# Optimization experiments

Hardware: AMD Instinct MI355X
Metric: run time of the kernel (lower is better)

Reference implementation:

```python
import jax, jax.numpy as jnp
import numpy as np

B, S, H, NH, HD = 2, 2048, 2048, 16, 128
E, TOPK, I = 8, 2, 2048
EPS = 1e-5
ROPE_THETA = 10000.0


def setup_inputs() -> dict:
    key = jax.random.key(0)
    ks = jax.random.split(key, 11)
    s = 0.02
    return {
        "hidden_states": jax.random.normal(ks[0], (B, S, H), jnp.float32),
        "position_ids": jnp.broadcast_to(jnp.arange(S, dtype=jnp.int32), (B, S)),
        "rms1_w": jnp.ones((H,), jnp.float32),
        "rms2_w": jnp.ones((H,), jnp.float32),
        "q_w": jax.random.normal(ks[1], (H, H), jnp.float32) * s,
        "k_w": jax.random.normal(ks[2], (H, H), jnp.float32) * s,
        "v_w": jax.random.normal(ks[3], (H, H), jnp.float32) * s,
        "o_w": jax.random.normal(ks[4], (H, H), jnp.float32) * s,
        "router_w": jax.random.normal(ks[5], (H, E), jnp.float32) * s,
        "w1": jax.random.normal(ks[6], (E, H, I), jnp.float32) * s,
        "w2": jax.random.normal(ks[7], (E, I, H), jnp.float32) * s,
        "w3": jax.random.normal(ks[8], (E, H, I), jnp.float32) * s,
    }


def rmsnorm(x, w):
    var = jnp.mean(x * x, axis=-1, keepdims=True)
    return (x * jax.lax.rsqrt(var + EPS)) * w


def rope(x, pos):
    # x: [B,S,NH,HD], pos: [B,S]
    half = HD // 2
    inv_freq = 1.0 / (ROPE_THETA ** (jnp.arange(0, half, dtype=jnp.float32) / half))
    ang = pos.astype(jnp.float32)[..., None] * inv_freq  # [B,S,half]
    cos = jnp.cos(ang)[:, :, None, :]
    sin = jnp.sin(ang)[:, :, None, :]
    x1, x2 = x[..., :half], x[..., half:]
    return jnp.concatenate([x1 * cos - x2 * sin, x2 * cos + x1 * sin], axis=-1)


def attention(x, pos, q_w, k_w, v_w, o_w):
    q = (x @ q_w).reshape(B, S, NH, HD)
    k = (x @ k_w).reshape(B, S, NH, HD)
    v = (x @ v_w).reshape(B, S, NH, HD)
    q = rope(q, pos)
    k = rope(k, pos)
    scores = jnp.einsum("bqhd,bkhd->bhqk", q, k) / np.sqrt(HD).astype(np.float32)
    causal = jnp.tril(jnp.ones((S, S), bool))
    scores = jnp.where(causal, scores, jnp.finfo(scores.dtype).min)
    probs = jax.nn.softmax(scores, axis=-1)
    ctx = jnp.einsum("bhqk,bkhd->bqhd", probs, v).reshape(B, S, H)
    return ctx @ o_w


def moe(x, router_w, w1, w2, w3):
    t = x.reshape(B * S, H)
    probs = jax.nn.softmax(t @ router_w, axis=-1)  # [T,E]
    top_v, top_i = jax.lax.top_k(probs, TOPK)
    top_v = top_v / jnp.sum(top_v, axis=-1, keepdims=True)
    T = B * S
    coeff = jnp.zeros((T, E), x.dtype).at[jnp.arange(T)[:, None], top_i].set(top_v)
    y = jnp.zeros((T, H), x.dtype)
    for e in range(E):  # fixed small expert loop
        h = jax.nn.silu(t @ w1[e]) * (t @ w3[e])
        y = y + coeff[:, e:e + 1] * (h @ w2[e])
    return y.reshape(B, S, H)


def reference(hidden_states, position_ids, rms1_w, rms2_w, q_w, k_w, v_w, o_w,
              router_w, w1, w2, w3):
    residual = hidden_states
    h = rmsnorm(hidden_states, rms1_w).astype(hidden_states.dtype)
    h = attention(h, position_ids, q_w, k_w, v_w, o_w)
    h = residual + h
    residual = h
    h = rmsnorm(h, rms2_w).astype(h.dtype)
    h = moe(h, router_w, w1, w2, w3)
    return residual + h
```

## Files before the change

### kernel.cpp

```cpp
#include <hip/hip_runtime.h>
#include <hip/hip_bf16.h>

constexpr int CB   = 2;
constexpr int CS   = 2048;
constexpr int CH   = 2048;
constexpr int CNH  = 16;
constexpr int CHD  = 128;
constexpr int CE   = 8;
constexpr int CI   = 2048;
constexpr int CT   = CB * CS;
constexpr int CQKV = 3 * CH;

typedef __attribute__((ext_vector_type(8))) short short8;
typedef __attribute__((ext_vector_type(4))) float float4v;
typedef __attribute__((ext_vector_type(4))) unsigned short ushort4v;
typedef unsigned int uint32;

__device__ __forceinline__ float bf2f(unsigned short u) {
    union { unsigned int i; float f; } x; x.i = ((unsigned int)u) << 16; return x.f;
}
__device__ __forceinline__ unsigned short f2bf(float f) {
    union { float f; unsigned int i; } x; x.f = f;
    unsigned int r = x.i + 0x7fffu + ((x.i >> 16) & 1u);
    return (unsigned short)(r >> 16);
}
__device__ __forceinline__ uint32 packpair(uint32 r0, uint32 r1) {
    return __builtin_amdgcn_perm(r1, r0, 0x07060302u);
}
__device__ __forceinline__ uint32 rnebits(float f) {
    uint32 u = __float_as_uint(f);
    return u + 0x7fffu + ((u >> 16) & 1u);
}
__device__ __forceinline__ void split2(float f0, float f1, uint32& h, uint32& l) {
    uint32 r0 = rnebits(f0), r1 = rnebits(f1);
    h = packpair(r0, r1);
    float d0 = f0 - __uint_as_float(r0 & 0xffff0000u);
    float d1 = f1 - __uint_as_float(r1 & 0xffff0000u);
    l = packpair(rnebits(d0), rnebits(d1));
}
__device__ __forceinline__ void rne16_store(const float* fv, unsigned short* dst) {
    uint32 h[8];
    #pragma unroll
    for (int p = 0; p < 8; p++) h[p] = packpair(rnebits(fv[2 * p]), rnebits(fv[2 * p + 1]));
    ((uint4*)dst)[0] = make_uint4(h[0], h[1], h[2], h[3]);
    ((uint4*)dst)[1] = make_uint4(h[4], h[5], h[6], h[7]);
}
__device__ __forceinline__ void gl16(const void* g, void* l) {
    __builtin_amdgcn_global_load_lds(
        (const __attribute__((address_space(1))) void*)g,
        (__attribute__((address_space(3))) void*)l, 16, 0, 0);
}

__global__ __launch_bounds__(256) void rmsnorm_k(const float* __restrict__ x,
                                                 const float* __restrict__ w,
                                                 unsigned short* __restrict__ o1,
                                                 unsigned short* __restrict__ o2) {
    const int row = blockIdx.x;
    const float* xr = x + (size_t)row * CH;
    const int base = threadIdx.x * 8;
    float4 v0 = *(const float4*)(xr + base);
    float4 v1 = *(const float4*)(xr + base + 4);
    float ss = v0.x*v0.x + v0.y*v0.y + v0.z*v0.z + v0.w*v0.w
             + v1.x*v1.x + v1.y*v1.y + v1.z*v1.z + v1.w*v1.w;
    #pragma unroll
    for (int o = 1; o < 64; o <<= 1) ss += __shfl_xor(ss, o);
    __shared__ float ps[4];
    if ((threadIdx.x & 63) == 0) ps[threadIdx.x >> 6] = ss;
    __syncthreads();
    const float scale = rsqrtf((ps[0] + ps[1] + ps[2] + ps[3]) / (float)CH + 1e-5f);
    float4 w0 = *(const float4*)(w + base);
    float4 w1 = *(const float4*)(w + base + 4);
    float r[8] = {v0.x * scale * w0.x, v0.y * scale * w0.y, v0.z * scale * w0.z, v0.w * scale * w0.w,
                  v1.x * scale * w1.x, v1.y * scale * w1.y, v1.z * scale * w1.z, v1.w * scale * w1.w};
    uint32 h[4], l[4];
    #pragma unroll
    for (int p = 0; p < 4; p++) split2(r[2 * p], r[2 * p + 1], h[p], l[p]);
    *(uint4*)(o1 + (size_t)row * CH + base) = make_uint4(h[0], h[1], h[2], h[3]);
    *(uint4*)(o2 + (size_t)row * CH + base) = make_uint4(l[0], l[1], l[2], l[3]);
}

__global__ __launch_bounds__(256) void rmsrouter_k(const float* __restrict__ x,
                                                   const float* __restrict__ w,
                                                   const float* __restrict__ rw,
                                                   unsigned short* __restrict__ h2,
                                                   int* __restrict__ cnt,
                                                   int* __restrict__ tok,
                                                   float* __restrict__ gate) {
    const int row = blockIdx.x;
    const float* xr = x + (size_t)row * CH;
    const int base = threadIdx.x * 8;
    float4 v0 = *(const float4*)(xr + base);
    float4 v1 = *(const float4*)(xr + base + 4);
    float ss = v0.x*v0.x + v0.y*v0.y + v0.z*v0.z + v0.w*v0.w
             + v1.x*v1.x + v1.y*v1.y + v1.z*v1.z + v1.w*v1.w;
    #pragma unroll
    for (int o = 1; o < 64; o <<= 1) ss += __shfl_xor(ss, o);
    __shared__ float ps[4];
    __shared__ double dacc[4][8];
    const int wave = threadIdx.x >> 6, lane = threadIdx.x & 63;
    if (lane == 0) ps[wave] = ss;
    __syncthreads();
    const float scale = rsqrtf((ps[0] + ps[1] + ps[2] + ps[3]) / (float)CH + 1e-5f);
    float4 w0 = *(const float4*)(w + base);
    float4 w1 = *(const float4*)(w + base + 4);
    float r[8] = {v0.x * scale * w0.x, v0.y * scale * w0.y, v0.z * scale * w0.z, v0.w * scale * w0.w,
                  v1.x * scale * w1.x, v1.y * scale * w1.y, v1.z * scale * w1.z, v1.w * scale * w1.w};
    rne16_store(r, h2 + (size_t)row * CH + base);
    const float vv[8] = {v0.x, v0.y, v0.z, v0.w, v1.x, v1.y, v1.z, v1.w};
    const float ww[8] = {w0.x, w0.y, w0.z, w0.w, w1.x, w1.y, w1.z, w1.w};
    double acc[8] = {0, 0, 0, 0, 0, 0, 0, 0};
    #pragma unroll
    for (int jj = 0; jj < 8; jj++) {
        const double xn = (double)vv[jj] * (double)ww[jj];
        const float* rr = rw + (size_t)(base + jj) * CE;
        #pragma unroll
        for (int e = 0; e < 8; e++) acc[e] += xn * (double)rr[e];
    }
    #pragma unroll
    for (int e = 0; e < 8; e++) {
        #pragma unroll
        for (int o = 1; o < 64; o <<= 1) acc[e] += __shfl_xor(acc[e], o);
    }
    if (lane == 0) {
        #pragma unroll
        for (int e = 0; e < 8; e++) dacc[wave][e] = acc[e];
    }
    __syncthreads();
    if (threadIdx.x == 0) {
        double a[8];
        #pragma unroll
        for (int e = 0; e < 8; e++) a[e] = dacc[0][e] + dacc[1][e] + dacc[2][e] + dacc[3][e];
        int e0 = 0;
        #pragma unroll
        for (int e = 1; e < 8; e++) if (a[e] > a[e0]) e0 = e;
        int e1 = (e0 == 0) ? 1 : 0;
        #pragma unroll
        for (int e = 0; e < 8; e++) if (e != e0 && a[e] > a[e1]) e1 = e;
        const double dl = (double)scale * (a[e1] - a[e0]);
        const double p1r = exp(dl);
        const float g0 = (float)(1.0 / (1.0 + p1r));
        const float g1 = (float)(p1r / (1.0 + p1r));
        int pos0 = atomicAdd(&cnt[e0], 1);
        tok[e0 * 4096 + pos0] = row; gate[e0 * 4096 + pos0] = g0;
        int pos1 = atomicAdd(&cnt[e1], 1);
        tok[e1 * 4096 + pos1] = row; gate[e1 * 4096 + pos1] = g1;
    }
}

__global__ void rope_tab_k(float2* __restrict__ tab) {
    int i = blockIdx.x * 256 + threadIdx.x;
    int p = i >> 6, j = i & 63;
    double inv = pow(10000.0, -(double)j / 64.0);
    float invf = (float)inv;
    float angf = (float)p * invf;
    double da = (double)angf;
    tab[i] = make_float2((float)cos(da), (float)sin(da));
}

__global__ __launch_bounds__(256) void rope_k(unsigned short* __restrict__ qh,
                                              unsigned short* __restrict__ ql,
                                              const int* __restrict__ pos,
                                              const float2* __restrict__ tab) {
    int i = blockIdx.x * 256 + threadIdx.x;
    if (i >= CT * CNH * 8) return;
    int t = i >> 7, r = i & 127, hh = r >> 3, jo = (r & 7) << 3;
    const float2* tp = tab + (size_t)pos[t] * 64 + jo;
    float4 tc0 = ((const float4*)tp)[0];
    float4 tc1 = ((const float4*)tp)[1];
    float4 tc2 = ((const float4*)tp)[2];
    float4 tc3 = ((const float4*)tp)[3];
    float cx[8] = {tc0.x, tc0.z, tc1.x, tc1.z, tc2.x, tc2.z, tc3.x, tc3.z};
    float cy[8] = {tc0.y, tc0.w, tc1.y, tc1.w, tc2.y, tc2.w, tc3.y, tc3.w};
    const size_t off = (size_t)t * CQKV + hh * CHD + jo;
    #pragma unroll
    for (int s = 0; s < 2; s++) {
        unsigned short* hp = qh + off + s * CH;
        unsigned short* lp = ql + off + s * CH;
        short8 x1h = *(short8*)hp,        x1l = *(short8*)lp;
        short8 x2h = *(short8*)(hp + 64), x2l = *(short8*)(lp + 64);
        const unsigned short* p1h = (const unsigned short*)&x1h;
        const unsigned short* p1l = (const unsigned short*)&x1l;
        const unsigned short* p2h = (const unsigned short*)&x2h;
        const unsigned short* p2l = (const unsigned short*)&x2l;
        short8 y1h, y1l, y2h, y2l;
        unsigned short* q1h = (unsigned short*)&y1h;
        unsigned short* q1l = (unsigned short*)&y1l;
        unsigned short* q2h = (unsigned short*)&y2h;
        unsigned short* q2l = (unsigned short*)&y2l;
        #pragma unroll
        for (int jj = 0; jj < 8; jj++) {
            const float x1 = bf2f(p1h[jj]) + bf2f(p1l[jj]);
            const float x2 = bf2f(p2h[jj]) + bf2f(p2l[jj]);
            const float yy1 = x1 * cx[jj] - x2 * cy[jj];
            const float yy2 = x2 * cx[jj] + x1 * cy[jj];
            const uint32 r1 = rnebits(yy1), r2 = rnebits(yy2);
            q1h[jj] = (unsigned short)(r1 >> 16);
            q2h[jj] = (unsigned short)(r2 >> 16);
            q1l[jj] = f2bf(yy1 - __uint_as_float(r1 & 0xffff0000u));
            q2l[jj] = f2bf(yy2 - __uint_as_float(r2 & 0xffff0000u));
        }
        *(short8*)hp        = y1h;
        *(short8*)(hp + 64) = y2h;
        *(short8*)lp        = y1l;
        *(short8*)(lp + 64) = y2l;
    }
}

template<int NMAT>
__global__ __launch_bounds__(256) void conv_k(const float* __restrict__ S0,
                                              const float* __restrict__ S1,
                                              unsigned short* __restrict__ D) {
    __shared__ float t[64][65];
    const int n0 = blockIdx.x * 64, k0 = blockIdx.y * 64, e = blockIdx.z;
    const size_t esrc = (size_t)e * 2048 * 2048;
    const int cc = threadIdx.x & 63, r4 = threadIdx.x >> 6;
    const int nl = threadIdx.x >> 2, q = threadIdx.x & 3;
    #pragma unroll
    for (int s = 0; s < NMAT; s++) {
        const float* S = s ? S1 : S0;
        __syncthreads();
        #pragma unroll
        for (int j = 0; j < 16; j++) {
            const int row = j * 4 + r4;
            t[cc][row] = S[esrc + (size_t)(k0 + row) * 2048 + n0 + cc];
        }
        __syncthreads();
        const int orow = (NMAT == 2) ? (2 * (n0 + nl) + s) : (n0 + nl);
        unsigned short* dp = D + (size_t)e * (NMAT * 2048) * 2048 + (size_t)orow * 2048 + k0 + q * 16;
        float fv[16];
        #pragma unroll
        for (int j = 0; j < 16; j++) fv[j] = t[nl][q * 16 + j];
        rne16_store(fv, dp);
    }
}

template<int NMAT>
__global__ __launch_bounds__(256) void convs_k(const float* __restrict__ S0,
                                               const float* __restrict__ S1,
                                               const float* __restrict__ S2,
                                               unsigned short* __restrict__ Dh,
                                               unsigned short* __restrict__ Dl) {
    __shared__ float t[64][65];
    const int n0 = blockIdx.x * 64, k0 = blockIdx.y * 64, z = blockIdx.z;
    const float* S = S0;
    if (NMAT == 3) S = (z == 0) ? S0 : ((z == 1) ? S1 : S2);
    const int cc = threadIdx.x & 63, r4 = threadIdx.x >> 6;
    #pragma unroll
    for (int j = 0; j < 16; j++) {
        const int row = j * 4 + r4;
        t[cc][row] = S[(size_t)(k0 + row) * 2048 + n0 + cc];
    }
    __syncthreads();
    const int nl = threadIdx.x >> 2, q = threadIdx.x & 3;
    float fv[16];
    #pragma unroll
    for (int j = 0; j < 16; j++) fv[j] = t[nl][q * 16 + j];
    uint32 h[8], l[8];
    #pragma unroll
    for (int p = 0; p < 8; p++) split2(fv[2 * p], fv[2 * p + 1], h[p], l[p]);
    const size_t off = (size_t)(z * 2048 + n0 + nl) * 2048 + k0 + q * 16;
    ((uint4*)(Dh + off))[0] = make_uint4(h[0], h[1], h[2], h[3]);
    ((uint4*)(Dh + off))[1] = make_uint4(h[4], h[5], h[6], h[7]);
    ((uint4*)(Dl + off))[0] = make_uint4(l[0], l[1], l[2], l[3]);
    ((uint4*)(Dl + off))[1] = make_uint4(l[4], l[5], l[6], l[7]);
}

template<int MODE>
__global__ __launch_bounds__(256) void sgemm_k(
    const unsigned short* __restrict__ Ahg, const unsigned short* __restrict__ Alg, int lda,
    const unsigned short* __restrict__ Bhg, const unsigned short* __restrict__ Blg, int K,
    unsigned short* __restrict__ Ch, unsigned short* __restrict__ Cl,
    float* __restrict__ Cf, int ldc,
    const float* __restrict__ resid, float* __restrict__ C2) {
    __shared__ unsigned short SS[2][4][128 * 32];
    const int mt = blockIdx.x, nt = blockIdx.y, tid = threadIdx.x;
    const int m0 = mt * 128;
    const int wave = tid >> 6, lane = tid & 63;
    const int lr = lane & 15, lg = lane >> 4;
    const int wr = (tid >> 7) & 1, wc = (tid >> 6) & 1;
    const int sr = lane >> 2;
    const int sc = (lane & 3) * 8;
    const int r0 = wave * 32;
    const int lofs = r0 * 32;
    const unsigned short* gAh = Ahg + (size_t)(m0 + r0 + sr) * lda + sc;
    const unsigned short* gAl = Alg + (size_t)(m0 + r0 + sr) * lda + sc;
    const unsigned short* gBh = Bhg + (size_t)(nt * 128 + r0 + sr) * K + sc;
    const unsigned short* gBl = Blg + (size_t)(nt * 128 + r0 + sr) * K + sc;
    const size_t rstepA = (size_t)16 * lda, rstepB = (size_t)16 * K;

    float4v acc[4][4];
    #pragma unroll
    for (int m = 0; m < 4; m++)
        #pragma unroll
        for (int n = 0; n < 4; n++) acc[m][n] = (float4v){0.f, 0.f, 0.f, 0.f};

    gl16(gAh, &SS[0][0][lofs]);           gl16(gAh + rstepA, &SS[0][0][lofs + 512]);
    gl16(gAl, &SS[0][1][lofs]);           gl16(gAl + rstepA, &SS[0][1][lofs + 512]);
    gl16(gBh, &SS[0][2][lofs]);           gl16(gBh + rstepB, &SS[0][2][lofs + 512]);
    gl16(gBl, &SS[0][3][lofs]);           gl16(gBl + rstepB, &SS[0][3][lofs + 512]);
    __syncthreads();

    int cur = 0;
    for (int k0 = 0; k0 < K; k0 += 32) {
        if (k0 + 32 < K) {
            const int nb = cur ^ 1;
            const int kn = k0 + 32;
            gl16(gAh + kn, &SS[nb][0][lofs]);          gl16(gAh + kn + rstepA, &SS[nb][0][lofs + 512]);
            gl16(gAl + kn, &SS[nb][1][lofs]);          gl16(gAl + kn + rstepA, &SS[nb][1][lofs + 512]);
            gl16(gBh + kn, &SS[nb][2][lofs]);          gl16(gBh + kn + rstepB, &SS[nb][2][lofs + 512]);
            gl16(gBl + kn, &SS[nb][3][lofs]);          gl16(gBl + kn + rstepB, &SS[nb][3][lofs + 512]);
        }
        const unsigned short* PAh = SS[cur][0];
        const unsigned short* PAl = SS[cur][1];
        const unsigned short* PBh = SS[cur][2];
        const unsigned short* PBl = SS[cur][3];
        short8 fah[4], fal[4], fbh[4], fbl[4];
        #pragma unroll
        for (int m = 0; m < 4; m++) {
            fah[m] = *(const short8*)(PAh + (wr * 64 + m * 16 + lr) * 32 + lg * 8);
            fal[m] = *(const short8*)(PAl + (wr * 64 + m * 16 + lr) * 32 + lg * 8);
        }
        #pragma unroll
        for (int n = 0; n < 4; n++) {
            fbh[n] = *(const short8*)(PBh + (wc * 64 + n * 16 + lr) * 32 + lg * 8);
            fbl[n] = *(const short8*)(PBl + (wc * 64 + n * 16 + lr) * 32 + lg * 8);
        }
        #pragma unroll
        for (int n = 0; n < 4; n++)
            #pragma unroll
            for (int m = 0; m < 4; m++) {
                acc[m][n] = __builtin_amdgcn_mfma_f32_16x16x32_bf16(fal[m], fbh[n], acc[m][n], 0, 0, 0);
                acc[m][n] = __builtin_amdgcn_mfma_f32_16x16x32_bf16(fah[m], fbl[n], acc[m][n], 0, 0, 0);
                acc[m][n] = __builtin_amdgcn_mfma_f32_16x16x32_bf16(fah[m], fbh[n], acc[m][n], 0, 0, 0);
            }
        __syncthreads();
        cur ^= 1;
    }
    #pragma unroll
    for (int m = 0; m < 4; m++) {
        const int rb = wr * 64 + m * 16 + (lane >> 4) * 4;
        #pragma unroll
        for (int n = 0; n < 4; n++) {
            const int ccol = nt * 128 + wc * 64 + n * 16 + lr;
            #pragma unroll
            for (int r = 0; r < 4; r++) {
                const size_t idx = (size_t)(m0 + rb + r) * ldc + ccol;
                if (MODE == 1) {
                    const float v = acc[m][n][r] + resid[idx];
                    Cf[idx] = v;
                    C2[idx] = v;
                } else {
                    const float v = acc[m][n][r];
                    uint32 rr = rnebits(v);
                    Ch[idx] = (unsigned short)(rr >> 16);
                    Cl[idx] = f2bf(v - __uint_as_float(rr & 0xffff0000u));
                }
            }
        }
    }
}

template<int MODE>
__global__ __launch_bounds__(256) void gemm_k(
    const unsigned short* __restrict__ A, int lda,
    const unsigned short* __restrict__ Bt, int K, int Ne,
    void* __restrict__ Cp, int ldc,
    const int* __restrict__ cnt, const int* __restrict__ tokl,
    const float* __restrict__ gatel, const int* __restrict__ pb) {
    __shared__ unsigned short SS[2][2][128 * 32];
    const int nt = blockIdx.x, mt = blockIdx.y, e = blockIdx.z;
    const int m0 = mt * 128;
    const int c = cnt[e];
    if (m0 >= c) return;
    const int valid = (c - m0 < 128) ? (c - m0) : 128;
    const int tid = threadIdx.x;
    const int wave = tid >> 6, lane = tid & 63;
    const int lr = lane & 15;
    const int wr = (tid >> 7) & 1, wc = (tid >> 6) & 1;
    const int sr = lane >> 2, sc = (lane & 3) * 8;
    const int r0 = wave * 32;
    const int lofs = r0 * 32;
    size_t gr0, gr1;
    {
        int ra = r0 + sr, rb2 = r0 + 16 + sr;
        if (MODE == 2) {
            ra = ra < valid ? ra : valid - 1;
            rb2 = rb2 < valid ? rb2 : valid - 1;
            gr0 = (size_t)tokl[e * 4096 + m0 + ra];
            gr1 = (size_t)tokl[e * 4096 + m0 + rb2];
        } else {
            int x0 = m0 + ra, x1 = m0 + rb2;
            gr0 = (size_t)(pb[e] + (x0 < c ? x0 : c - 1));
            gr1 = (size_t)(pb[e] + (x1 < c ? x1 : c - 1));
        }
    }
    const unsigned short* gA0 = A + gr0 * (size_t)lda + sc;
    const unsigned short* gA1 = A + gr1 * (size_t)lda + sc;
    const unsigned short* gB = Bt + (size_t)e * Ne * K + (size_t)(nt * 128 + r0 + sr) * K + sc;
    const size_t rstepB = (size_t)16 * K;

    float4v acc[4][4];
    #pragma unroll
    for (int m = 0; m < 4; m++)
        #pragma unroll
        for (int n = 0; n < 4; n++) acc[m][n] = (float4v){0.f, 0.f, 0.f, 0.f};

    gl16(gA0, &SS[0][0][lofs]);           gl16(gA1, &SS[0][0][lofs + 512]);
    gl16(gB, &SS[0][1][lofs]);            gl16(gB + rstepB, &SS[0][1][lofs + 512]);
    __syncthreads();

    int cur = 0;
    for (int k0 = 0; k0 < K; k0 += 32) {
        if (k0 + 32 < K) {
            const int nb = cur ^ 1;
            const int kn = k0 + 32;
            gl16(gA0 + kn, &SS[nb][0][lofs]);          gl16(gA1 + kn, &SS[nb][0][lofs + 512]);
            gl16(gB + kn, &SS[nb][1][lofs]);           gl16(gB + kn + rstepB, &SS[nb][1][lofs + 512]);
        }
        const unsigned short* PA = SS[cur][0];
        const unsigned short* PB = SS[cur][1];
        short8 af[4], bf[4];
        const int lg = lane >> 4;
        #pragma unroll
        for (int m = 0; m < 4; m++) af[m] = *(const short8*)(PA + (wr * 64 + m * 16 + lr) * 32 + lg * 8);
        #pragma unroll
        for (int n = 0; n < 4; n++) bf[n] = *(const short8*)(PB + (wc * 64 + n * 16 + lr) * 32 + lg * 8);
        #pragma unroll
        for (int n = 0; n < 4; n++)
            #pragma unroll
            for (int m = 0; m < 4; m++)
                acc[m][n] = __builtin_amdgcn_mfma_f32_16x16x32_bf16(af[m], bf[n], acc[m][n], 0, 0, 0);
        __syncthreads();
        cur ^= 1;
    }

    #pragma unroll
    for (int m = 0; m < 4; m++) {
        const int rb = wr * 64 + m * 16 + (lane >> 4) * 4;
        #pragma unroll
        for (int n = 0; n < 4; n++) {
            const int col = nt * 128 + wc * 64 + n * 16 + lr;
            #pragma unroll
            for (int r = 0; r < 4; r++) {
                const int row = rb + r;
                const float v = acc[m][n][r];
                if (MODE == 2) {
                    const float other = __shfl_xor(v, 1);
                    if (!(lr & 1) && row < valid) {
                        const float g1 = v, g3 = other;
                        const float hsw = (g1 / (1.f + __expf(-g1))) * g3;
                        ((unsigned short*)Cp)[(size_t)(pb[e] + m0 + row) * ldc + (col >> 1)] = f2bf(hsw);
                    }
                } else {
                    if (row < valid) {
                        const int t = tokl[e * 4096 + m0 + row];
                        const float g = gatel[e * 4096 + m0 + row];
                        atomicAdd(((float*)Cp) + (size_t)t * ldc + col, v * g);
                    }
                }
            }
        }
    }
}

__global__ __launch_bounds__(256) void attn_k(const unsigned short* __restrict__ qh,
                                              const unsigned short* __restrict__ ql,
                                              unsigned short* __restrict__ ch,
                                              unsigned short* __restrict__ cl) {
    __shared__ unsigned short Ksh[32][136], Ksl[32][136];
    __shared__ unsigned short Vth[128][40], Vtl[128][40];
    const int bid = blockIdx.x;
    const int xcd = bid & 7, jj = bid >> 3;
    const int bh  = xcd * 4 + (jj >> 5);
    const int qb  = 31 - (jj & 31);
    const int h   = bh & 15, b = bh >> 4;
    const int tid = threadIdx.x;
    const int wave = tid >> 6, lane = tid & 63, lr = lane & 15, lg = lane >> 4;
    const size_t tb = (size_t)b * CS;
    const int q0 = qb * 64 + wave * 16;

    short8 qfh[4], qfl[4];
    {
        const size_t off = (tb + q0 + lr) * CQKV + h * CHD;
        #pragma unroll
        for (int c = 0; c < 4; c++) {
            qfh[c] = *(const short8*)(qh + off + c * 32 + lg * 8);
            qfl[c] = *(const short8*)(ql + off + c * 32 + lg * 8);
        }
    }
    float4v o[8];
    #pragma unroll
    for (int d = 0; d < 8; d++) o[d] = (float4v){0.f, 0.f, 0.f, 0.f};
    float m = -1e30f, l = 0.f;
    const float scl = 0.08838834764831845f;
    const int ntiles = 2 * (qb + 1);
    const int kk = tid >> 3, slot = tid & 7;
    const int vd = tid & 127, vhalf = tid >> 7;

    short8 pkh0, pkh1, pkl0, pkl1;
    unsigned short pth[16], ptl[16];
    {
        const size_t koff = (tb + kk) * CQKV + CH + h * CHD + slot * 16;
        pkh0 = *(const short8*)(qh + koff);
        pkh1 = *(const short8*)(qh + koff + 8);
        pkl0 = *(const short8*)(ql + koff);
        pkl1 = *(const short8*)(ql + koff + 8);
        const size_t voff = (tb + vhalf * 16) * CQKV + 2 * CH + h * CHD + vd;
        #pragma unroll
        for (int j = 0; j < 16; j++) {
            pth[j] = qh[voff + (size_t)j * CQKV];
            ptl[j] = ql[voff + (size_t)j * CQKV];
        }
    }

    for (int kt = 0; kt < ntiles; ++kt) {
        const int kv0 = kt * 32;
        __syncthreads();
        *(short8*)(&Ksh[kk][slot * 16])     = pkh0;
        *(short8*)(&Ksh[kk][slot * 16 + 8]) = pkh1;
        *(short8*)(&Ksl[kk][slot * 16])     = pkl0;
        *(short8*)(&Ksl[kk][slot * 16 + 8]) = pkl1;
        #pragma unroll
        for (int p = 0; p < 2; p++) {
            *(ushort4v*)(&Vth[vd][vhalf * 16 + p * 8])     = *(ushort4v*)(&pth[p * 8]);
            *(ushort4v*)(&Vth[vd][vhalf * 16 + p * 8 + 4]) = *(ushort4v*)(&pth[p * 8 + 4]);
            *(ushort4v*)(&Vtl[vd][vhalf * 16 + p * 8])     = *(ushort4v*)(&ptl[p * 8]);
            *(ushort4v*)(&Vtl[vd][vhalf * 16 + p * 8 + 4]) = *(ushort4v*)(&ptl[p * 8 + 4]);
        }
        if (kt + 1 < ntiles) {
            const int nv0 = kv0 + 32;
            const size_t koff = (tb + nv0 + kk) * CQKV + CH + h * CHD + slot * 16;
            pkh0 = *(const short8*)(qh + koff);
            pkh1 = *(const short8*)(qh + koff + 8);
            pkl0 = *(const short8*)(ql + koff);
            pkl1 = *(const short8*)(ql + koff + 8);
            const size_t voff = (tb + nv0 + vhalf * 16) * CQKV + 2 * CH + h * CHD + vd;
            #pragma unroll
            for (int j = 0; j < 16; j++) {
                pth[j] = qh[voff + (size_t)j * CQKV];
                ptl[j] = ql[voff + (size_t)j * CQKV];
            }
        }
        __syncthreads();

        float4v st0 = (float4v){0.f,0.f,0.f,0.f}, st1 = st0;
        #pragma unroll
        for (int c = 0; c < 4; c++) {
            short8 kah = *(const short8*)(&Ksh[lr][c * 32 + lg * 8]);
            short8 kal = *(const short8*)(&Ksl[lr][c * 32 + lg * 8]);
            short8 kbh = *(const short8*)(&Ksh[16 + lr][c * 32 + lg * 8]);
            short8 kbl = *(const short8*)(&Ksl[16 + lr][c * 32 + lg * 8]);
            st0 = __builtin_amdgcn_mfma_f32_16x16x32_bf16(kal, qfh[c], st0, 0, 0, 0);
            st0 = __builtin_amdgcn_mfma_f32_16x16x32_bf16(kah, qfl[c], st0, 0, 0, 0);
            st0 = __builtin_amdgcn_mfma_f32_16x16x32_bf16(kah, qfh[c], st0, 0, 0, 0);
            st1 = __builtin_amdgcn_mfma_f32_16x16x32_bf16(kbl, qfh[c], st1, 0, 0, 0);
            st1 = __builtin_amdgcn_mfma_f32_16x16x32_bf16(kbh, qfl[c], st1, 0, 0, 0);
            st1 = __builtin_amdgcn_mfma_f32_16x16x32_bf16(kbh, qfh[c], st1, 0, 0, 0);
        }
        float pv[8]; float pmax = -1e30f;
        const int qg = q0 + lr;
        #pragma unroll
        for (int f = 0; f < 2; f++) {
            #pragma unroll
            for (int r = 0; r < 4; r++) {
                const int kg = kv0 + f * 16 + lg * 4 + r;
                const float s = (kg <= qg) ? ((f ? st1[r] : st0[r]) * scl) : -1e30f;
                pv[f * 4 + r] = s;
                pmax = fmaxf(pmax, s);
            }
        }
        pmax = fmaxf(pmax, __shfl_xor(pmax, 16));
        pmax = fmaxf(pmax, __shfl_xor(pmax, 32));
        if (!__all(pmax <= m)) {
            const float mnew = fmaxf(m, pmax);
            const float alpha = __expf(m - mnew);
            l *= alpha;
            #pragma unroll
            for (int d = 0; d < 8; d++) o[d] *= alpha;
            m = mnew;
        }
        float sum = 0.f;
        #pragma unroll
        for (int i = 0; i < 8; i++) { const float p = __expf(pv[i] - m); pv[i] = p; sum += p; }
        sum += __shfl_xor(sum, 16);
        sum += __shfl_xor(sum, 32);
        l += sum;
        short8 pfh, pfl;
        unsigned short* pfhp = (unsigned short*)&pfh;
        unsigned short* pflp = (unsigned short*)&pfl;
        #pragma unroll
        for (int j = 0; j < 8; j++) {
            const int srcl = (((lg & 1) * 2 + (j >> 2)) << 4) | lr;
            const float a0 = __shfl(pv[j & 3], srcl);
            const float a1 = __shfl(pv[4 + (j & 3)], srcl);
            const float sel = (lg >= 2) ? a1 : a0;
            uint32 r = rnebits(sel);
            pfhp[j] = (unsigned short)(r >> 16);
            float d = sel - __uint_as_float(r & 0xffff0000u);
            pflp[j] = (unsigned short)(rnebits(d) >> 16);
        }
        #pragma unroll
        for (int dt = 0; dt < 8; dt++) {
            short8 vh = *(const short8*)(&Vth[dt * 16 + lr][lg * 8]);
            short8 vl = *(const short8*)(&Vtl[dt * 16 + lr][lg * 8]);
            o[dt] = __builtin_amdgcn_mfma_f32_16x16x32_bf16(vl, pfh, o[dt], 0, 0, 0);
            o[dt] = __builtin_amdgcn_mfma_f32_16x16x32_bf16(vh, pfl, o[dt], 0, 0, 0);
            o[dt] = __builtin_amdgcn_mfma_f32_16x16x32_bf16(vh, pfh, o[dt], 0, 0, 0);
        }
    }
    const float inv = 1.f / l;
    const size_t coff = (tb + q0 + lr) * CH + h * CHD + lg * 4;
    #pragma unroll
    for (int dt = 0; dt < 8; dt++) {
        ushort4v wh, wl;
        #pragma unroll
        for (int r = 0; r < 4; r++) {
            const float v = o[dt][r] * inv;
            uint32 rr = rnebits(v);
            wh[r] = (unsigned short)(rr >> 16);
            wl[r] = f2bf(v - __uint_as_float(rr & 0xffff0000u));
        }
        *(ushort4v*)(ch + coff + dt * 16) = wh;
        *(ushort4v*)(cl + coff + dt * 16) = wl;
    }
}

__global__ void prefix_k(const int* __restrict__ cnt, int* __restrict__ pb) {
    if (threadIdx.x == 0 && blockIdx.x == 0) {
        int s = 0;
        for (int e = 0; e < CE; e++) { pb[e] = s; s += cnt[e]; }
    }
}

extern "C" void kernel_launch(void* const* d_in, const int* in_sizes, int n_in,
                              void* d_out, int out_size, void* d_ws, size_t ws_size,
                              hipStream_t stream) {
    (void)in_sizes; (void)n_in; (void)out_size; (void)ws_size;
    const float* hidden = (const float*)d_in[0];
    const int*   posids = (const int*)d_in[1];
    const float* rms1w  = (const float*)d_in[2];
    const float* rms2w  = (const float*)d_in[3];
    const float* qw     = (const float*)d_in[4];
    const float* kw     = (const float*)d_in[5];
    const float* vw     = (const float*)d_in[6];
    const float* ow     = (const float*)d_in[7];
    const float* rw     = (const float*)d_in[8];
    const float* w1     = (const float*)d_in[9];
    const float* w2     = (const float*)d_in[10];
    const float* w3     = (const float*)d_in[11];
    float* out = (float*)d_out;

    char* ws = (char*)d_ws;
    unsigned short* h1h = (unsigned short*)ws;
    unsigned short* h1l = (unsigned short*)(ws + 16777216);
    unsigned short* woh = (unsigned short*)ws;
    unsigned short* wol = (unsigned short*)(ws + 8388608);
    unsigned short* h2  = (unsigned short*)ws;
    int*   tok  = (int*)(ws + 16777216);
    float* gate = (float*)(ws + 16777216 + 131072);
    int*   cnt  = (int*)(ws + 16777216 + 262144);
    int*   pb   = cnt + 16;
    unsigned short* qkvh = (unsigned short*)(ws + 33554432);
    unsigned short* qkvl = (unsigned short*)(ws + 83886080);
    unsigned short* wt13 = (unsigned short*)(ws + 33554432);
    unsigned short* wt2  = (unsigned short*)(ws + 33554432);
    unsigned short* wqkvh = (unsigned short*)(ws + 134217728);
    unsigned short* wqkvl = (unsigned short*)(ws + 134217728 + 25165824);
    unsigned short* ctxh = (unsigned short*)(ws + 134217728);
    unsigned short* ctxl = (unsigned short*)(ws + 150994944);
    float*          res2 = (float*)(ws + 167772160);
    unsigned short* Hbuf = (unsigned short*)(ws + 167772160);
    float2*         rtab = (float2*)(ws + 201326592);

    rope_tab_k<<<512, 256, 0, stream>>>(rtab);
    rmsnorm_k<<<CT, 256, 0, stream>>>(hidden, rms1w, h1h, h1l);
    convs_k<3><<<dim3(32, 32, 3), 256, 0, stream>>>(qw, kw, vw, wqkvh, wqkvl);
    sgemm_k<0><<<dim3(32, 48), 256, 0, stream>>>(h1h, h1l, CH, wqkvh, wqkvl, CH,
                                                 qkvh, qkvl, nullptr, CQKV, nullptr, nullptr);
    rope_k<<<2048, 256, 0, stream>>>(qkvh, qkvl, posids, rtab);
    convs_k<1><<<dim3(32, 32, 1), 256, 0, stream>>>(ow, nullptr, nullptr, woh, wol);
    attn_k<<<1024, 256, 0, stream>>>(qkvh, qkvl, ctxh, ctxl);
    sgemm_k<1><<<dim3(32, 16), 256, 0, stream>>>(ctxh, ctxl, CH, woh, wol, CH,
                                                 nullptr, nullptr, res2, CH, hidden, out);
    hipMemsetAsync(cnt, 0, 8 * sizeof(int), stream);
    rmsrouter_k<<<CT, 256, 0, stream>>>(res2, rms2w, rw, h2, cnt, tok, gate);
    prefix_k<<<1, 64, 0, stream>>>(cnt, pb);
    conv_k<2><<<dim3(32, 32, CE), 256, 0, stream>>>(w1, w3, wt13);
    gemm_k<2><<<dim3(32, 32, CE), 256, 0, stream>>>(h2, CH, wt13, CH, 2 * CI, Hbuf, CI,
                                                    cnt, tok, gate, pb);
    conv_k<1><<<dim3(32, 32, CE), 256, 0, stream>>>(w2, nullptr, wt2);
    gemm_k<3><<<dim3(16, 32, CE), 256, 0, stream>>>(Hbuf, CI, wt2, CI, CH, out, CH,
                                                    cnt, tok, gate, pb);
}
```

Before: 1.315 ms.

## Write V transposed from QKV GEMM and double-buffer K/V tiles in attention

The QKV GEMM epilogue now writes V in a transposed [dim][token] layout into separate buffers, while Q and K stay in a packed 4096-wide array. The attention kernel loads the V tiles directly into shared memory with async global-to-LDS copies, replacing the strided per-element gather and transpose it used before. K and V tiles are double-buffered in shared memory, so the next tile is prefetched while the current one is computed, cutting one barrier per iteration. The cost is a strided transposed store in the GEMM epilogue and a larger shared-memory footprint, which may lower occupancy.

```diff
diff --git a/kernel.cpp b/kernel.cpp
--- a/kernel.cpp
+++ b/kernel.cpp
@@ -9,7 +9,7 @@
 constexpr int CE   = 8;
 constexpr int CI   = 2048;
 constexpr int CT   = CB * CS;
-constexpr int CQKV = 3 * CH;
+constexpr int CQK  = 4096;
 
 typedef __attribute__((ext_vector_type(8))) short short8;
 typedef __attribute__((ext_vector_type(4))) float float4v;
@@ -171,7 +171,7 @@
     float4 tc3 = ((const float4*)tp)[3];
     float cx[8] = {tc0.x, tc0.z, tc1.x, tc1.z, tc2.x, tc2.z, tc3.x, tc3.z};
     float cy[8] = {tc0.y, tc0.w, tc1.y, tc1.w, tc2.y, tc2.w, tc3.y, tc3.w};
-    const size_t off = (size_t)t * CQKV + hh * CHD + jo;
+    const size_t off = (size_t)t * CQK + hh * CHD + jo;
     #pragma unroll
     for (int s = 0; s < 2; s++) {
         unsigned short* hp = qh + off + s * CH;
@@ -271,7 +271,8 @@
     const unsigned short* __restrict__ Bhg, const unsigned short* __restrict__ Blg, int K,
     unsigned short* __restrict__ Ch, unsigned short* __restrict__ Cl,
     float* __restrict__ Cf, int ldc,
-    const float* __restrict__ resid, float* __restrict__ C2) {
+    const float* __restrict__ resid, float* __restrict__ C2,
+    unsigned short* __restrict__ Vh, unsigned short* __restrict__ Vl) {
     __shared__ unsigned short SS[2][4][128 * 32];
     const int mt = blockIdx.x, nt = blockIdx.y, tid = threadIdx.x;
     const int m0 = mt * 128;
@@ -336,9 +337,30 @@
         __syncthreads();
         cur ^= 1;
     }
+    if (MODE == 0 && nt >= 32) {
+        #pragma unroll
+        for (int m = 0; m < 4; m++) {
+            const int rb = wr * 64 + m * 16 + lg * 4;
+            #pragma unroll
+            for (int n = 0; n < 4; n++) {
+                const int vcol = nt * 128 + wc * 64 + n * 16 + lr - 4096;
+                ushort4v wh4, wl4;
+                #pragma unroll
+                for (int r = 0; r < 4; r++) {
+                    const float v = acc[m][n][r];
+                    uint32 rr = rnebits(v);
+                    wh4[r] = (unsigned short)(rr >> 16);
+                    wl4[r] = f2bf(v - __uint_as_float(rr & 0xffff0000u));
+                }
+                *(ushort4v*)(Vh + (size_t)vcol * (size_t)CT + (m0 + rb)) = wh4;
+                *(ushort4v*)(Vl + (size_t)vcol * (size_t)CT + (m0 + rb)) = wl4;
+            }
+        }
+        return;
+    }
     #pragma unroll
     for (int m = 0; m < 4; m++) {
-        const int rb = wr * 64 + m * 16 + (lane >> 4) * 4;
+        const int rb = wr * 64 + m * 16 + lg * 4;
         #pragma unroll
         for (int n = 0; n < 4; n++) {
             const int ccol = nt * 128 + wc * 64 + n * 16 + lr;
@@ -463,12 +485,14 @@
     }
 }
 
-__global__ __launch_bounds__(256) void attn_k(const unsigned short* __restrict__ qh,
-                                              const unsigned short* __restrict__ ql,
+__global__ __launch_bounds__(256) void attn_k(const unsigned short* __restrict__ qkh,
+                                              const unsigned short* __restrict__ qkl,
+                                              const unsigned short* __restrict__ vth,
+                                              const unsigned short* __restrict__ vtl,
                                               unsigned short* __restrict__ ch,
                                               unsigned short* __restrict__ cl) {
-    __shared__ unsigned short Ksh[32][136], Ksl[32][136];
-    __shared__ unsigned short Vth[128][40], Vtl[128][40];
+    __shared__ unsigned short Kb[2][2][32][136];
+    __shared__ unsigned short Vb[2][2][128 * 32];
     const int bid = blockIdx.x;
     const int xcd = bid & 7, jj = bid >> 3;
     const int bh  = xcd * 4 + (jj >> 5);
@@ -481,11 +505,11 @@
 
     short8 qfh[4], qfl[4];
     {
-        const size_t off = (tb + q0 + lr) * CQKV + h * CHD;
+        const size_t off = (tb + q0 + lr) * CQK + h * CHD;
         #pragma unroll
         for (int c = 0; c < 4; c++) {
-            qfh[c] = *(const short8*)(qh + off + c * 32 + lg * 8);
-            qfl[c] = *(const short8*)(ql + off + c * 32 + lg * 8);
+            qfh[c] = *(const short8*)(qkh + off + c * 32 + lg * 8);
+            qfl[c] = *(const short8*)(qkl + off + c * 32 + lg * 8);
         }
     }
     float4v o[8];
@@ -495,61 +519,54 @@
     const float scl = 0.08838834764831845f;
     const int ntiles = 2 * (qb + 1);
     const int kk = tid >> 3, slot = tid & 7;
-    const int vd = tid & 127, vhalf = tid >> 7;
-
-    short8 pkh0, pkh1, pkl0, pkl1;
-    unsigned short pth[16], ptl[16];
-    {
-        const size_t koff = (tb + kk) * CQKV + CH + h * CHD + slot * 16;
-        pkh0 = *(const short8*)(qh + koff);
-        pkh1 = *(const short8*)(qh + koff + 8);
-        pkl0 = *(const short8*)(ql + koff);
-        pkl1 = *(const short8*)(ql + koff + 8);
-        const size_t voff = (tb + vhalf * 16) * CQKV + 2 * CH + h * CHD + vd;
-        #pragma unroll
-        for (int j = 0; j < 16; j++) {
-            pth[j] = qh[voff + (size_t)j * CQKV];
-            ptl[j] = ql[voff + (size_t)j * CQKV];
-        }
-    }
-
+
+    short8 kh0, kh1, kl0, kl1;
+    const size_t vrow = (size_t)(h * 128 + wave * 32 + (lane >> 2));
+    const unsigned short* gV0 = vth + vrow * (size_t)CT + tb + (lane & 3) * 8;
+    const unsigned short* gV1 = vtl + vrow * (size_t)CT + tb + (lane & 3) * 8;
+
+    #define LOADK(KV0) { \
+        const size_t koff = (tb + (KV0) + kk) * CQK + CH + h * CHD + slot * 16; \
+        kh0 = *(const short8*)(qkh + koff);     kh1 = *(const short8*)(qkh + koff + 8); \
+        kl0 = *(const short8*)(qkl + koff);     kl1 = *(const short8*)(qkl + koff + 8); }
+    #define WRITEK(BUF) { \
+        *(short8*)(&Kb[BUF][0][kk][slot * 16])     = kh0; \
+        *(short8*)(&Kb[BUF][0][kk][slot * 16 + 8]) = kh1; \
+        *(short8*)(&Kb[BUF][1][kk][slot * 16])     = kl0; \
+        *(short8*)(&Kb[BUF][1][kk][slot * 16 + 8]) = kl1; }
+    #define ISSUEV(BUF, KV0) { \
+        gl16(gV0 + (KV0), &Vb[BUF][0][wave * 32 * 32]); \
+        gl16(gV0 + (KV0) + (size_t)16 * CT, &Vb[BUF][0][wave * 32 * 32 + 512]); \
+        gl16(gV1 + (KV0), &Vb[BUF][1][wave * 32 * 32]); \
+        gl16(gV1 + (KV0) + (size_t)16 * CT, &Vb[BUF][1][wave * 32 * 32 + 512]); }
+
+    LOADK(0);
+    WRITEK(0);
+    ISSUEV(0, 0);
+    LOADK(32);
+    __syncthreads();
+
+    int cur = 0;
     for (int kt = 0; kt < ntiles; ++kt) {
         const int kv0 = kt * 32;
-        __syncthreads();
-        *(short8*)(&Ksh[kk][slot * 16])     = pkh0;
-        *(short8*)(&Ksh[kk][slot * 16 + 8]) = pkh1;
-        *(short8*)(&Ksl[kk][slot * 16])     = pkl0;
-        *(short8*)(&Ksl[kk][slot * 16 + 8]) = pkl1;
-        #pragma unroll
-        for (int p = 0; p < 2; p++) {
-            *(ushort4v*)(&Vth[vd][vhalf * 16 + p * 8])     = *(ushort4v*)(&pth[p * 8]);
-            *(ushort4v*)(&Vth[vd][vhalf * 16 + p * 8 + 4]) = *(ushort4v*)(&pth[p * 8 + 4]);
-            *(ushort4v*)(&Vtl[vd][vhalf * 16 + p * 8])     = *(ushort4v*)(&ptl[p * 8]);
-            *(ushort4v*)(&Vtl[vd][vhalf * 16 + p * 8 + 4]) = *(ushort4v*)(&ptl[p * 8 + 4]);
-        }
         if (kt + 1 < ntiles) {
-            const int nv0 = kv0 + 32;
-            const size_t koff = (tb + nv0 + kk) * CQKV + CH + h * CHD + slot * 16;
-            pkh0 = *(const short8*)(qh + koff);
-            pkh1 = *(const short8*)(qh + koff + 8);
-            pkl0 = *(const short8*)(ql + koff);
-            pkl1 = *(const short8*)(ql + koff + 8);
-            const size_t voff = (tb + nv0 + vhalf * 16) * CQKV + 2 * CH + h * CHD + vd;
-            #pragma unroll
-            for (int j = 0; j < 16; j++) {
-                pth[j] = qh[voff + (size_t)j * CQKV];
-                ptl[j] = ql[voff + (size_t)j * CQKV];
-            }
-        }
-        __syncthreads();
+            WRITEK(cur ^ 1);
+            ISSUEV(cur ^ 1, kv0 + 32);
+        }
+        if (kt + 2 < ntiles) LOADK(kv0 + 64);
+
+        const unsigned short* KH = &Kb[cur][0][0][0];
+        const unsigned short* KL = &Kb[cur][1][0][0];
+        const unsigned short* VH = Vb[cur][0];
+        const unsigned short* VL = Vb[cur][1];
 
         float4v st0 = (float4v){0.f,0.f,0.f,0.f}, st1 = st0;
         #pragma unroll
         for (int c = 0; c < 4; c++) {
-            short8 kah = *(const short8*)(&Ksh[lr][c * 32 + lg * 8]);
-            short8 kal = *(const short8*)(&Ksl[lr][c * 32 + lg * 8]);
-            short8 kbh = *(const short8*)(&Ksh[16 + lr][c * 32 + lg * 8]);
-            short8 kbl = *(const short8*)(&Ksl[16 + lr][c * 32 + lg * 8]);
+            short8 kah = *(const short8*)(KH + lr * 136 + c * 32 + lg * 8);
+            short8 kal = *(const short8*)(KL + lr * 136 + c * 32 + lg * 8);
+            short8 kbh = *(const short8*)(KH + (16 + lr) * 136 + c * 32 + lg * 8);
+            short8 kbl = *(const short8*)(KL + (16 + lr) * 136 + c * 32 + lg * 8);
             st0 = __builtin_amdgcn_mfma_f32_16x16x32_bf16(kal, qfh[c], st0, 0, 0, 0);
             st0 = __builtin_amdgcn_mfma_f32_16x16x32_bf16(kah, qfl[c], st0, 0, 0, 0);
             st0 = __builtin_amdgcn_mfma_f32_16x16x32_bf16(kah, qfh[c], st0, 0, 0, 0);
@@ -601,13 +618,18 @@
         }
         #pragma unroll
         for (int dt = 0; dt < 8; dt++) {
-            short8 vh = *(const short8*)(&Vth[dt * 16 + lr][lg * 8]);
-            short8 vl = *(const short8*)(&Vtl[dt * 16 + lr][lg * 8]);
+            short8 vh = *(const short8*)(VH + (dt * 16 + lr) * 32 + lg * 8);
+            short8 vl = *(const short8*)(VL + (dt * 16 + lr) * 32 + lg * 8);
             o[dt] = __builtin_amdgcn_mfma_f32_16x16x32_bf16(vl, pfh, o[dt], 0, 0, 0);
             o[dt] = __builtin_amdgcn_mfma_f32_16x16x32_bf16(vh, pfl, o[dt], 0, 0, 0);
             o[dt] = __builtin_amdgcn_mfma_f32_16x16x32_bf16(vh, pfh, o[dt], 0, 0, 0);
         }
-    }
+        __syncthreads();
+        cur ^= 1;
+    }
+    #undef LOADK
+    #undef WRITEK
+    #undef ISSUEV
     const float inv = 1.f / l;
     const size_t coff = (tb + q0 + lr) * CH + h * CHD + lg * 4;
     #pragma unroll
@@ -660,8 +682,10 @@
     float* gate = (float*)(ws + 16777216 + 131072);
     int*   cnt  = (int*)(ws + 16777216 + 262144);
     int*   pb   = cnt + 16;
-    unsigned short* qkvh = (unsigned short*)(ws + 33554432);
-    unsigned short* qkvl = (unsigned short*)(ws + 83886080);
+    unsigned short* qkh = (unsigned short*)(ws + 33554432);
+    unsigned short* qkl = (unsigned short*)(ws + 67108864);
+    unsigned short* vth = (unsigned short*)(ws + 100663296);
+    unsigned short* vtl = (unsigned short*)(ws + 117440512);
     unsigned short* wt13 = (unsigned short*)(ws + 33554432);
     unsigned short* wt2  = (unsigned short*)(ws + 33554432);
     unsigned short* wqkvh = (unsigned short*)(ws + 134217728);
@@ -676,12 +700,14 @@
     rmsnorm_k<<<CT, 256, 0, stream>>>(hidden, rms1w, h1h, h1l);
     convs_k<3><<<dim3(32, 32, 3), 256, 0, stream>>>(qw, kw, vw, wqkvh, wqkvl);
     sgemm_k<0><<<dim3(32, 48), 256, 0, stream>>>(h1h, h1l, CH, wqkvh, wqkvl, CH,
-                                                 qkvh, qkvl, nullptr, CQKV, nullptr, nullptr);
-    rope_k<<<2048, 256, 0, stream>>>(qkvh, qkvl, posids, rtab);
+                                                 qkh, qkl, nullptr, CQK, nullptr, nullptr,
+                                                 vth, vtl);
+    rope_k<<<2048, 256, 0, stream>>>(qkh, qkl, posids, rtab);
     convs_k<1><<<dim3(32, 32, 1), 256, 0, stream>>>(ow, nullptr, nullptr, woh, wol);
-    attn_k<<<1024, 256, 0, stream>>>(qkvh, qkvl, ctxh, ctxl);
+    attn_k<<<1024, 256, 0, stream>>>(qkh, qkl, vth, vtl, ctxh, ctxl);
     sgemm_k<1><<<dim3(32, 16), 256, 0, stream>>>(ctxh, ctxl, CH, woh, wol, CH,
-                                                 nullptr, nullptr, res2, CH, hidden, out);
+                                                 nullptr, nullptr, res2, CH, hidden, out,
+                                                 nullptr, nullptr);
     hipMemsetAsync(cnt, 0, 8 * sizeof(int), stream);
     rmsrouter_k<<<CT, 256, 0, stream>>>(res2, rms2w, rw, h2, cnt, tok, gate);
     prefix_k<<<1, 64, 0, stream>>>(cnt, pb);
```

After: 1.286 ms. 2.2% less time.
